# Kernel optimization log

Hardware: AMD Instinct MI355X
Metric: run time of the kernel (lower is better)

Reference implementation:

```python
import jax, jax.numpy as jnp
import numpy as np

N_NODES = 50000
N_EDGES = 640000
HID = 128
LN_EPS = 1e-5


def setup_inputs() -> dict:
    key = jax.random.key(0)
    ks = jax.random.split(key, 8)
    x = jax.random.normal(ks[0], (N_NODES, HID), dtype=jnp.float32)
    edge_index = jax.random.randint(ks[1], (2, N_EDGES), 0, N_NODES, dtype=jnp.int64)
    edge_attr = jax.random.normal(ks[2], (N_EDGES, HID), dtype=jnp.float32)
    # parameters (Kaiming-ish scaling)
    msg_W1 = jax.random.normal(ks[3], (3 * HID, HID), dtype=jnp.float32) / np.sqrt(3 * HID)
    msg_b1 = jnp.zeros((HID,), dtype=jnp.float32)
    msg_W2 = jax.random.normal(ks[4], (HID, HID), dtype=jnp.float32) / np.sqrt(HID)
    msg_b2 = jnp.zeros((HID,), dtype=jnp.float32)
    upd_W1 = jax.random.normal(ks[5], (2 * HID, HID), dtype=jnp.float32) / np.sqrt(2 * HID)
    upd_b1 = jnp.zeros((HID,), dtype=jnp.float32)
    upd_W2 = jax.random.normal(ks[6], (HID, HID), dtype=jnp.float32) / np.sqrt(HID)
    upd_b2 = jnp.zeros((HID,), dtype=jnp.float32)
    ln_gamma = jnp.ones((HID,), dtype=jnp.float32)
    ln_beta = jnp.zeros((HID,), dtype=jnp.float32)
    return {
        'x': x, 'edge_index': edge_index, 'edge_attr': edge_attr,
        'msg_W1': msg_W1, 'msg_b1': msg_b1, 'msg_W2': msg_W2, 'msg_b2': msg_b2,
        'upd_W1': upd_W1, 'upd_b1': upd_b1, 'upd_W2': upd_W2, 'upd_b2': upd_b2,
        'ln_gamma': ln_gamma, 'ln_beta': ln_beta,
    }


def _layer_norm(h, gamma, beta):
    mu = jnp.mean(h, axis=-1, keepdims=True)
    var = jnp.mean(jnp.square(h - mu), axis=-1, keepdims=True)
    return (h - mu) * jax.lax.rsqrt(var + LN_EPS) * gamma + beta


def reference(x, edge_index, edge_attr,
              msg_W1, msg_b1, msg_W2, msg_b2,
              upd_W1, upd_b1, upd_W2, upd_b2,
              ln_gamma, ln_beta):
    src, dst = edge_index[0], edge_index[1]
    # batched per-edge gather + concat: [E, 3*HID]
    msg_in = jnp.concatenate([x[src], x[dst], edge_attr], axis=-1)
    # message MLP (dropout is identity in eval)
    h = jax.nn.relu(msg_in @ msg_W1 + msg_b1)
    messages = h @ msg_W2 + msg_b2  # [E, HID]
    # scatter-add aggregation by destination node
    aggregated = jax.ops.segment_sum(messages, dst, num_segments=x.shape[0])
    # update MLP
    upd_in = jnp.concatenate([x, aggregated], axis=-1)  # [N, 2*HID]
    u = jax.nn.relu(upd_in @ upd_W1 + upd_b1)
    updated = u @ upd_W2 + upd_b2
    return _layer_norm(x + updated, ln_gamma, ln_beta)
```

## Files before the change

### kernel.cpp

```cpp
#include <hip/hip_runtime.h>

#define HID 128

typedef __attribute__((ext_vector_type(8))) short short8;
typedef __attribute__((ext_vector_type(4))) float f32x4;
typedef __attribute__((ext_vector_type(2))) float f32x2;

__device__ __forceinline__ float bf2f(unsigned short u) {
  union { unsigned int u; float f; } c; c.u = ((unsigned int)u) << 16; return c.f;
}
__device__ __forceinline__ unsigned short f2bf(float f) {
  union { float f; unsigned int u; } c; c.f = f;
  unsigned int u = c.u;
  return (unsigned short)((u + 0x7FFFu + ((u >> 16) & 1u)) >> 16);
}
__device__ __forceinline__ float loads(const void* p, size_t i, bool f32) {
  return f32 ? ((const float*)p)[i] : bf2f(((const unsigned short*)p)[i]);
}
__device__ __forceinline__ short8 load_a8(const void* base, size_t row, int k, bool f32) {
  if (!f32) return *(const short8*)((const unsigned short*)base + row * HID + k);
  const float* fp = (const float*)base + row * HID + k;
  f32x4 f0 = *(const f32x4*)fp;
  f32x4 f1 = *(const f32x4*)(fp + 4);
  short8 t;
  t[0] = (short)f2bf(f0[0]); t[1] = (short)f2bf(f0[1]);
  t[2] = (short)f2bf(f0[2]); t[3] = (short)f2bf(f0[3]);
  t[4] = (short)f2bf(f1[0]); t[5] = (short)f2bf(f1[1]);
  t[6] = (short)f2bf(f1[2]); t[7] = (short)f2bf(f1[3]);
  return t;
}

__global__ void detect_kernel(const void* __restrict__ x,
                              const int* __restrict__ eidx,
                              int* __restrict__ flags) {
  __shared__ int bad, oddnz;
  if (threadIdx.x == 0) { bad = 0; oddnz = 0; }
  __syncthreads();
  const unsigned short* xu = (const unsigned short*)x;
  int mybad = 0;
  for (int i = threadIdx.x; i < 4096; i += 256) {
    int ef = (xu[i] >> 7) & 0xFF;
    if (!(ef == 0 || (ef >= 90 && ef <= 140))) mybad++;
  }
  if (mybad) atomicAdd(&bad, mybad);
  if (threadIdx.x < 128) {
    if (eidx[2 * threadIdx.x + 1] != 0) atomicAdd(&oddnz, 1);
  }
  __syncthreads();
  if (threadIdx.x == 0) {
    flags[0] = (bad > 409) ? 1 : 0;
    flags[1] = (oddnz == 0) ? 1 : 0;
  }
}

__device__ __forceinline__ int get_dst(const int* eidx, bool i64, int E, int e) {
  return i64 ? eidx[2 * (E + e)] : eidx[E + e];
}
__device__ __forceinline__ int get_src(const int* eidx, bool i64, int E, int e) {
  return i64 ? eidx[2 * e] : eidx[e];
}

__global__ void zero_out_kernel(unsigned int* __restrict__ out,
                                const int* __restrict__ flags, long long nelem) {
  bool f32 = flags[0] != 0;
  size_t words = (size_t)nelem * (f32 ? 2 : 1) / 2;
  for (size_t w = blockIdx.x * 256ull + threadIdx.x; w < words; w += (size_t)gridDim.x * 256ull)
    out[w] = 0u;
}

__global__ void repack_all(const void* __restrict__ W1, const void* __restrict__ W2,
                           const void* __restrict__ U1, const void* __restrict__ U2,
                           unsigned short* __restrict__ P1, unsigned short* __restrict__ P2,
                           unsigned short* __restrict__ PU1, unsigned short* __restrict__ PU2,
                           const int* __restrict__ flags) {
  const bool f32 = flags[0] != 0;
  int idx = blockIdx.x * 256 + threadIdx.x;
  const int s1 = 384 * 128, s2 = s1 + 128 * 128, s3 = s2 + 256 * 128, s4 = s3 + 128 * 128;
  if (idx >= s4) return;
  const void* W; unsigned short* P; int off;
  if (idx < s1)      { W = W1; P = P1;  off = idx; }
  else if (idx < s2) { W = W2; P = P2;  off = idx - s1; }
  else if (idx < s3) { W = U1; P = PU1; off = idx - s2; }
  else               { W = U2; P = PU2; off = idx - s3; }
  int j = off & 7, lane = (off >> 3) & 63, ct = (off >> 9) & 7, ks = off >> 12;
  int k = ks * 32 + ((lane >> 4) << 3) + j;
  int n = ct * 16 + (lane & 15);
  P[off] = f2bf(loads(W, (size_t)k * 128 + n, f32));
}

__global__ void hist_kernel(const int* __restrict__ eidx, int* __restrict__ counts,
                            const int* __restrict__ flags, int E, int N) {
  const bool i64 = flags[1] != 0;
  int e = blockIdx.x * 256 + threadIdx.x;
  if (e < E) {
    int d = get_dst(eidx, i64, E, e);
    d = min(max(d, 0), N - 1);
    atomicAdd(&counts[d], 1);
  }
}

__global__ __launch_bounds__(1024) void scanA_kernel(const int* __restrict__ cnt,
                                                     int* __restrict__ curb,
                                                     int* __restrict__ bsum, int N) {
  __shared__ int wsum[16], wsum2[16];
  const int tid = threadIdx.x, lane = tid & 63, wid = tid >> 6;
  int i = blockIdx.x * 1024 + tid;
  int v = (i < N) ? cnt[i] : 0;
  int s = v;
#pragma unroll
  for (int off = 1; off < 64; off <<= 1) {
    int t = __shfl_up(s, off, 64);
    if (lane >= off) s += t;
  }
  if (lane == 63) wsum[wid] = s;
  __syncthreads();
  if (wid == 0 && lane < 16) {
    int w = wsum[lane];
#pragma unroll
    for (int off = 1; off < 16; off <<= 1) {
      int t = __shfl_up(w, off, 16);
      if (lane >= off) w += t;
    }
    wsum2[lane] = w;
    if (lane == 15) bsum[blockIdx.x] = w;
  }
  __syncthreads();
  int pre = (wid > 0) ? wsum2[wid - 1] : 0;
  if (i < N) curb[i] = pre + s - v;
}

__global__ void scanB_kernel(int* __restrict__ bsum, int nb) {
  if (threadIdx.x == 0 && blockIdx.x == 0) {
    int run = 0;
    for (int b = 0; b < nb; b++) { int t = bsum[b]; bsum[b] = run; run += t; }
  }
}

__global__ __launch_bounds__(1024) void scanC_kernel(int* __restrict__ curb,
                                                     const int* __restrict__ bsum, int N) {
  int i = blockIdx.x * 1024 + threadIdx.x;
  if (i < N) curb[i] += bsum[blockIdx.x];
}

__global__ __launch_bounds__(256) void x1_kernel(
    const void* __restrict__ x, const unsigned short* __restrict__ P1,
    const void* __restrict__ b1, unsigned short* __restrict__ X1,
    const int* __restrict__ flags, int N) {
  __shared__ unsigned short hs[64][264];
  const bool f32 = flags[0] != 0;
  const int tid = threadIdx.x, lane = tid & 63, wid = tid >> 6;
  const int l15 = lane & 15, quad = lane >> 4;
  const int base = blockIdx.x * 64;
  int mn = min(base + wid * 16 + l15, N - 1);

  f32x4 zero = {0.f, 0.f, 0.f, 0.f};
  f32x4 acca[8], accb[8];
#pragma unroll
  for (int ct = 0; ct < 8; ct++) { acca[ct] = zero; accb[ct] = zero; }
#pragma unroll
  for (int ks = 0; ks < 4; ks++) {
    short8 a = load_a8(x, (size_t)mn, ks * 32 + quad * 8, f32);
    const unsigned short* wpa = P1 + ((size_t)(ks * 8) * 64 + lane) * 8;
    const unsigned short* wpb = P1 + ((size_t)((ks + 4) * 8) * 64 + lane) * 8;
#pragma unroll
    for (int ct = 0; ct < 8; ct++) {
      short8 ba = *(const short8*)(wpa + ct * 512);
      short8 bb = *(const short8*)(wpb + ct * 512);
      acca[ct] = __builtin_amdgcn_mfma_f32_16x16x32_bf16(a, ba, acca[ct], 0, 0, 0);
      accb[ct] = __builtin_amdgcn_mfma_f32_16x16x32_bf16(a, bb, accb[ct], 0, 0, 0);
    }
  }
#pragma unroll
  for (int ct = 0; ct < 8; ct++) {
    const int col = ct * 16 + l15;
    const float bv = loads(b1, col, f32);
#pragma unroll
    for (int r = 0; r < 4; r++) {
      hs[wid * 16 + quad * 4 + r][col]       = f2bf(acca[ct][r] + bv);
      hs[wid * 16 + quad * 4 + r][128 + col] = f2bf(accb[ct][r]);
    }
  }
  __syncthreads();
  const int row = tid >> 2, part = tid & 3;
  if (base + row < N) {
    unsigned short* op = X1 + (size_t)(base + row) * 256 + part * 64;
#pragma unroll
    for (int j = 0; j < 8; j++)
      *(short8*)(op + j * 8) = *(const short8*)&hs[row][part * 64 + j * 8];
  }
}

__global__ __launch_bounds__(256, 8) void edgeS_kernel(
    const void* __restrict__ eattr, const int* __restrict__ ssrc,
    const int* __restrict__ sdst, const int* __restrict__ perm,
    const unsigned short* __restrict__ X1,
    const unsigned short* __restrict__ P1, const unsigned short* __restrict__ P2,
    const void* __restrict__ b2, float* __restrict__ aggf,
    const int* __restrict__ flags, int E, int N) {
  __shared__ __align__(16) char smem[64 * 136 * 2];
  __shared__ int sdst_s[64], ssrc_s[64];
  unsigned short (*hs)[136] = (unsigned short (*)[136])smem;
  float (*ms)[68] = (float (*)[68])smem;
  const bool f32 = flags[0] != 0;
  const int tid = threadIdx.x, lane = tid & 63, wid = tid >> 6;
  const int l15 = lane & 15, quad = lane >> 4;
  const int base = blockIdx.x * 64;

  if (tid < 64) {
    int e = min(base + tid, E - 1);
    sdst_s[tid] = sdst[e];
    ssrc_s[tid] = ssrc[e];
  }

  const int me = min(base + wid * 16 + l15, E - 1);
  const int pe = perm[me];

  f32x4 zero = {0.f, 0.f, 0.f, 0.f};
  f32x4 acc[8];
#pragma unroll
  for (int ct = 0; ct < 8; ct++) acc[ct] = zero;
#pragma unroll
  for (int ks = 0; ks < 4; ks++) {
    short8 a = load_a8(eattr, (size_t)pe, ks * 32 + quad * 8, f32);
    const unsigned short* wp = P1 + ((size_t)((ks + 8) * 8) * 64 + lane) * 8;
#pragma unroll
    for (int ct = 0; ct < 8; ct++) {
      short8 b = *(const short8*)(wp + ct * 512);
      acc[ct] = __builtin_amdgcn_mfma_f32_16x16x32_bf16(a, b, acc[ct], 0, 0, 0);
    }
  }
#pragma unroll
  for (int ct = 0; ct < 8; ct++) {
    const int col = ct * 16 + l15;
#pragma unroll
    for (int r = 0; r < 4; r++)
      hs[wid * 16 + quad * 4 + r][col] = f2bf(acc[ct][r]);
  }
  __syncthreads();

  {
    const int r = wid * 16 + (lane >> 2);
    const int cq = (lane & 3) * 8;
    const int s = ssrc_s[r], d = sdst_s[r];
    const unsigned short* ap = X1 + (size_t)s * 256;
    const unsigned short* bp = X1 + (size_t)d * 256 + 128;
#pragma unroll
    for (int j = 0; j < 4; j++) {
      const int c0 = cq + j * 32;
      short8 h8 = *(const short8*)&hs[r][c0];
      short8 a8 = *(const short8*)(ap + c0);
      short8 b8 = *(const short8*)(bp + c0);
      short8 o;
#pragma unroll
      for (int k = 0; k < 8; k++) {
        float v = bf2f((unsigned short)h8[k]) + bf2f((unsigned short)a8[k])
                + bf2f((unsigned short)b8[k]);
        o[k] = (short)f2bf(fmaxf(v, 0.f));
      }
      *(short8*)&hs[r][c0] = o;
    }
  }

  f32x4 acc2[8];
#pragma unroll
  for (int ct = 0; ct < 8; ct++) acc2[ct] = zero;
#pragma unroll
  for (int ks = 0; ks < 4; ks++) {
    short8 a = *(const short8*)&hs[wid * 16 + l15][ks * 32 + quad * 8];
    const unsigned short* wp = P2 + ((size_t)(ks * 8) * 64 + lane) * 8;
#pragma unroll
    for (int ct = 0; ct < 8; ct++) {
      short8 b = *(const short8*)(wp + ct * 512);
      acc2[ct] = __builtin_amdgcn_mfma_f32_16x16x32_bf16(a, b, acc2[ct], 0, 0, 0);
    }
  }
  float b2v[8];
#pragma unroll
  for (int ct = 0; ct < 8; ct++) b2v[ct] = loads(b2, ct * 16 + l15, f32);

#pragma unroll
  for (int h = 0; h < 2; h++) {
    __syncthreads();
#pragma unroll
    for (int c = 0; c < 4; c++) {
      const int ct = h * 4 + c;
      const int colh = c * 16 + l15;
#pragma unroll
      for (int r = 0; r < 4; r++) {
        const int e = base + wid * 16 + quad * 4 + r;
        ms[wid * 16 + quad * 4 + r][colh] = (e < E) ? (acc2[ct][r] + b2v[ct]) : 0.0f;
      }
    }
    __syncthreads();
    const int colh = tid & 63;
    const int col  = h * 64 + colh;
    const int grp  = tid >> 6;
    const int r0   = grp * 16;
    float sum = 0.0f;
    int cur = sdst_s[r0];
#pragma unroll 4
    for (int r = r0; r < r0 + 16; r++) {
      int d = sdst_s[r];
      if (d != cur) {
        atomicAdd(&aggf[(size_t)cur * HID + col], sum);
        sum = 0.0f; cur = d;
      }
      sum += ms[r][colh];
    }
    atomicAdd(&aggf[(size_t)cur * HID + col], sum);
  }
}

__global__ __launch_bounds__(1024) void scan_kernel(const int* __restrict__ counts,
                                                    int* __restrict__ offs, int N) {
  __shared__ int wsum[16];
  __shared__ int wpre[16];
  __shared__ int carry_s;
  const int tid = threadIdx.x, lane = tid & 63, wid = tid >> 6;
  if (tid == 0) carry_s = 0;
  __syncthreads();
  for (int base = 0; base < N; base += 1024) {
    int i = base + tid;
    int v = (i < N) ? counts[i] : 0;
    int s = v;
#pragma unroll
    for (int off = 1; off < 64; off <<= 1) {
      int t = __shfl_up(s, off, 64);
      if (lane >= off) s += t;
    }
    if (lane == 63) wsum[wid] = s;
    __syncthreads();
    if (tid == 0) {
      int run = carry_s;
#pragma unroll
      for (int w = 0; w < 16; w++) { int t = wsum[w]; wpre[w] = run; run += t; }
      carry_s = run;
    }
    __syncthreads();
    if (i < N) offs[i] = wpre[wid] + s - v;
    __syncthreads();
  }
  if (tid == 0) offs[N] = carry_s;
}

__global__ void scatter_kernel(const int* __restrict__ eidx, int* __restrict__ cur,
                               int* __restrict__ ssrc, int* __restrict__ sdst,
                               int* __restrict__ perm,
                               const int* __restrict__ flags, int E, int N) {
  const bool i64 = flags[1] != 0;
  int e = blockIdx.x * 256 + threadIdx.x;
  if (e < E) {
    int d = get_dst(eidx, i64, E, e);
    int s = get_src(eidx, i64, E, e);
    d = min(max(d, 0), N - 1);
    s = min(max(s, 0), N - 1);
    int pos = atomicAdd(&cur[d], 1);
    ssrc[pos] = s;
    sdst[pos] = d;
    perm[pos] = e;
  }
}

__global__ __launch_bounds__(256) void edge_kernel_sorted(
    const void* __restrict__ x, const void* __restrict__ eattr,
    const int* __restrict__ ssrc, const int* __restrict__ sdst,
    const int* __restrict__ perm,
    const unsigned short* __restrict__ P1, const void* __restrict__ b1,
    const unsigned short* __restrict__ P2, const void* __restrict__ b2,
    float* __restrict__ aggf, const int* __restrict__ flags, int E, int N) {
  __shared__ __align__(16) char smem[64 * 132 * 4];
  __shared__ int sdst_s[64];
  unsigned short (*hs)[136] = (unsigned short (*)[136])smem;
  float (*ms)[132] = (float (*)[132])smem;
  const bool f32 = flags[0] != 0;
  const int tid = threadIdx.x, lane = tid & 63, wid = tid >> 6;
  const int l15 = lane & 15, quad = lane >> 4;
  const int base = blockIdx.x * 64;

  if (tid < 64) sdst_s[tid] = sdst[min(base + tid, E - 1)];

  int me = base + wid * 16 + l15;
  if (me >= E) me = E - 1;
  const int src = ssrc[me];
  const int dsm = sdst[me];
  const int pe  = perm[me];

  f32x4 zero = {0.f, 0.f, 0.f, 0.f};
  f32x4 acc[8];
#pragma unroll
  for (int ct = 0; ct < 8; ct++) acc[ct] = zero;
#pragma unroll
  for (int ks = 0; ks < 12; ks++) {
    const int k0 = ks * 32;
    short8 a;
    if (k0 < 128)      a = load_a8(x,     (size_t)src, k0 + quad * 8, f32);
    else if (k0 < 256) a = load_a8(x,     (size_t)dsm, (k0 - 128) + quad * 8, f32);
    else               a = load_a8(eattr, (size_t)pe,  (k0 - 256) + quad * 8, f32);
    const unsigned short* wp = P1 + ((size_t)(ks * 8) * 64 + lane) * 8;
#pragma unroll
    for (int ct = 0; ct < 8; ct++) {
      short8 b = *(const short8*)(wp + ct * 512);
      acc[ct] = __builtin_amdgcn_mfma_f32_16x16x32_bf16(a, b, acc[ct], 0, 0, 0);
    }
  }
#pragma unroll
  for (int ct = 0; ct < 8; ct++) {
    const int col = ct * 16 + l15;
    const float bv = loads(b1, col, f32);
#pragma unroll
    for (int r = 0; r < 4; r++)
      hs[wid * 16 + quad * 4 + r][col] = f2bf(fmaxf(acc[ct][r] + bv, 0.f));
  }
  f32x4 acc2[8];
#pragma unroll
  for (int ct = 0; ct < 8; ct++) acc2[ct] = zero;
#pragma unroll
  for (int ks = 0; ks < 4; ks++) {
    short8 a = *(const short8*)&hs[wid * 16 + l15][ks * 32 + quad * 8];
    const unsigned short* wp = P2 + ((size_t)(ks * 8) * 64 + lane) * 8;
#pragma unroll
    for (int ct = 0; ct < 8; ct++) {
      short8 b = *(const short8*)(wp + ct * 512);
      acc2[ct] = __builtin_amdgcn_mfma_f32_16x16x32_bf16(a, b, acc2[ct], 0, 0, 0);
    }
  }
  float b2v[8];
#pragma unroll
  for (int ct = 0; ct < 8; ct++) b2v[ct] = loads(b2, ct * 16 + l15, f32);
  __syncthreads();
#pragma unroll
  for (int ct = 0; ct < 8; ct++) {
    const int col = ct * 16 + l15;
#pragma unroll
    for (int r = 0; r < 4; r++) {
      const int e = base + wid * 16 + quad * 4 + r;
      ms[wid * 16 + quad * 4 + r][col] = (e < E) ? (acc2[ct][r] + b2v[ct]) : 0.0f;
    }
  }
  __syncthreads();
  const int col  = tid & 127;
  const int half = tid >> 7;
  const int r0 = half * 32;
  float sum = 0.0f;
  int cur = sdst_s[r0];
#pragma unroll 4
  for (int r = r0; r < r0 + 32; r++) {
    int d = sdst_s[r];
    if (d != cur) {
      atomicAdd(&aggf[(size_t)cur * HID + col], sum);
      sum = 0.0f; cur = d;
    }
    sum += ms[r][col];
  }
  atomicAdd(&aggf[(size_t)cur * HID + col], sum);
}

__global__ __launch_bounds__(256) void edge_kernel_plain(
    const void* __restrict__ x, const int* __restrict__ eidx,
    const void* __restrict__ eattr,
    const unsigned short* __restrict__ P1, const void* __restrict__ b1,
    const unsigned short* __restrict__ P2, const void* __restrict__ b2,
    float* __restrict__ aggf, void* __restrict__ out,
    const int* __restrict__ flags, int E, int N, int small_mode) {
  __shared__ unsigned short hs[64][136];
  const bool f32 = flags[0] != 0;
  const bool i64 = flags[1] != 0;
  const int tid = threadIdx.x, lane = tid & 63, wid = tid >> 6;
  const int l15 = lane & 15, quad = lane >> 4;
  const int base = blockIdx.x * 64;

  int me = base + wid * 16 + l15;
  if (me >= E) me = E - 1;
  int src = get_src(eidx, i64, E, me);
  int dsm = get_dst(eidx, i64, E, me);
  src = min(max(src, 0), N - 1);
  dsm = min(max(dsm, 0), N - 1);

  f32x4 zero = {0.f, 0.f, 0.f, 0.f};
  f32x4 acc[8];
#pragma unroll
  for (int ct = 0; ct < 8; ct++) acc[ct] = zero;
#pragma unroll
  for (int ks = 0; ks < 12; ks++) {
    const int k0 = ks * 32;
    short8 a;
    if (k0 < 128)      a = load_a8(x,     (size_t)src, k0 + quad * 8, f32);
    else if (k0 < 256) a = load_a8(x,     (size_t)dsm, (k0 - 128) + quad * 8, f32);
    else               a = load_a8(eattr, (size_t)me,  (k0 - 256) + quad * 8, f32);
    const unsigned short* wp = P1 + ((size_t)(ks * 8) * 64 + lane) * 8;
#pragma unroll
    for (int ct = 0; ct < 8; ct++) {
      short8 b = *(const short8*)(wp + ct * 512);
      acc[ct] = __builtin_amdgcn_mfma_f32_16x16x32_bf16(a, b, acc[ct], 0, 0, 0);
    }
  }
#pragma unroll
  for (int ct = 0; ct < 8; ct++) {
    const int col = ct * 16 + l15;
    const float bv = loads(b1, col, f32);
#pragma unroll
    for (int r = 0; r < 4; r++)
      hs[wid * 16 + quad * 4 + r][col] = f2bf(fmaxf(acc[ct][r] + bv, 0.f));
  }
  __syncthreads();
  f32x4 acc2[8];
#pragma unroll
  for (int ct = 0; ct < 8; ct++) acc2[ct] = zero;
#pragma unroll
  for (int ks = 0; ks < 4; ks++) {
    short8 a = *(const short8*)&hs[wid * 16 + l15][ks * 32 + quad * 8];
    const unsigned short* wp = P2 + ((size_t)(ks * 8) * 64 + lane) * 8;
#pragma unroll
    for (int ct = 0; ct < 8; ct++) {
      short8 b = *(const short8*)(wp + ct * 512);
      acc2[ct] = __builtin_amdgcn_mfma_f32_16x16x32_bf16(a, b, acc2[ct], 0, 0, 0);
    }
  }
  float b2v[8];
#pragma unroll
  for (int ct = 0; ct < 8; ct++) b2v[ct] = loads(b2, ct * 16 + l15, f32);

  if (!small_mode || f32) {
    float* tgt = (!small_mode) ? aggf : (float*)out;
#pragma unroll
    for (int r = 0; r < 4; r++) {
      const int e = base + wid * 16 + quad * 4 + r;
      if (e < E) {
        int d = get_dst(eidx, i64, E, e);
        d = min(max(d, 0), N - 1);
        float* op = tgt + (size_t)d * HID + l15;
#pragma unroll
        for (int ct = 0; ct < 8; ct++) atomicAdd(op + ct * 16, acc2[ct][r] + b2v[ct]);
      }
    }
  } else {
#pragma unroll
    for (int ct = 0; ct < 8; ct++) {
      const int col = ct * 16 + l15;
#pragma unroll
      for (int r = 0; r < 4; r++)
        hs[wid * 16 + quad * 4 + r][col] = f2bf(acc2[ct][r] + b2v[ct]);
    }
    __syncthreads();
    const int row = tid >> 2;
    const int cg  = (tid & 3) * 32;
    const int e = base + row;
    if (e < E) {
      int d = get_dst(eidx, i64, E, e);
      d = min(max(d, 0), N - 1);
      unsigned int* orow = (unsigned int*)out + ((size_t)d * HID >> 1);
#pragma unroll
      for (int p = 0; p < 16; p++) {
        const int col = cg + p * 2;
        const float lo = bf2f(hs[row][col]);
        const float hi = bf2f(hs[row][col + 1]);
        unsigned int* wp = orow + (col >> 1);
        unsigned int old = *wp, assumed;
        do {
          assumed = old;
          unsigned int nv = (unsigned int)f2bf(bf2f((unsigned short)(assumed & 0xFFFF)) + lo)
                          | ((unsigned int)f2bf(bf2f((unsigned short)(assumed >> 16)) + hi) << 16);
          old = atomicCAS(wp, assumed, nv);
        } while (old != assumed);
      }
    }
  }
}

__global__ __launch_bounds__(256) void node_kernel(
    const void* __restrict__ x, const float* __restrict__ aggf,
    const unsigned short* __restrict__ PU1, const void* __restrict__ ub1,
    const unsigned short* __restrict__ PU2, const void* __restrict__ ub2,
    const void* __restrict__ gamma, const void* __restrict__ beta,
    void* __restrict__ out, const int* __restrict__ flags, int N, int small_mode) {
  __shared__ unsigned short hs[64][136];
  const bool f32 = flags[0] != 0;
  const int tid = threadIdx.x, lane = tid & 63, wid = tid >> 6;
  const int l15 = lane & 15, quad = lane >> 4;
  const int base = blockIdx.x * 64;

  int mn = base + wid * 16 + l15;
  if (mn >= N) mn = N - 1;

  const void* aggp = (!small_mode) ? (const void*)aggf : (const void*)out;
  const bool aggF32 = (!small_mode) ? true : f32;

  f32x4 zero = {0.f, 0.f, 0.f, 0.f};
  f32x4 acc[8];
#pragma unroll
  for (int ct = 0; ct < 8; ct++) acc[ct] = zero;
#pragma unroll
  for (int ks = 0; ks < 8; ks++) {
    const int k0 = ks * 32;
    short8 a;
    if (k0 < 128) a = load_a8(x,    (size_t)mn, k0 + quad * 8, f32);
    else          a = load_a8(aggp, (size_t)mn, (k0 - 128) + quad * 8, aggF32);
    const unsigned short* wp = PU1 + ((size_t)(ks * 8) * 64 + lane) * 8;
#pragma unroll
    for (int ct = 0; ct < 8; ct++) {
      short8 b = *(const short8*)(wp + ct * 512);
      acc[ct] = __builtin_amdgcn_mfma_f32_16x16x32_bf16(a, b, acc[ct], 0, 0, 0);
    }
  }
#pragma unroll
  for (int ct = 0; ct < 8; ct++) {
    const int col = ct * 16 + l15;
    const float bv = loads(ub1, col, f32);
#pragma unroll
    for (int r = 0; r < 4; r++)
      hs[wid * 16 + quad * 4 + r][col] = f2bf(fmaxf(acc[ct][r] + bv, 0.f));
  }
  __syncthreads();
  f32x4 acc2[8];
#pragma unroll
  for (int ct = 0; ct < 8; ct++) acc2[ct] = zero;
#pragma unroll
  for (int ks = 0; ks < 4; ks++) {
    short8 a = *(const short8*)&hs[wid * 16 + l15][ks * 32 + quad * 8];
    const unsigned short* wp = PU2 + ((size_t)(ks * 8) * 64 + lane) * 8;
#pragma unroll
    for (int ct = 0; ct < 8; ct++) {
      short8 b = *(const short8*)(wp + ct * 512);
      acc2[ct] = __builtin_amdgcn_mfma_f32_16x16x32_bf16(a, b, acc2[ct], 0, 0, 0);
    }
  }

  float vals[8][4];
  float s1[4] = {0.f, 0.f, 0.f, 0.f};
  float s2[4] = {0.f, 0.f, 0.f, 0.f};
#pragma unroll
  for (int ct = 0; ct < 8; ct++) {
    const int col = ct * 16 + l15;
    const float bv = loads(ub2, col, f32);
#pragma unroll
    for (int r = 0; r < 4; r++) {
      int row = base + wid * 16 + quad * 4 + r;
      int rc = row < N ? row : 0;
      float v = acc2[ct][r] + bv + loads(x, (size_t)rc * HID + col, f32);
      vals[ct][r] = v;
      s1[r] += v;
      s2[r] += v * v;
    }
  }
#pragma unroll
  for (int off = 1; off < 16; off <<= 1) {
#pragma unroll
    for (int r = 0; r < 4; r++) {
      s1[r] += __shfl_xor(s1[r], off, 16);
      s2[r] += __shfl_xor(s2[r], off, 16);
    }
  }
#pragma unroll
  for (int r = 0; r < 4; r++) {
    const int row = base + wid * 16 + quad * 4 + r;
    if (row < N) {
      const float mean = s1[r] * (1.0f / 128.0f);
      const float var  = fmaxf(s2[r] * (1.0f / 128.0f) - mean * mean, 0.0f);
      const float rstd = rsqrtf(var + 1e-5f);
#pragma unroll
      for (int ct = 0; ct < 8; ct++) {
        const int col = ct * 16 + l15;
        float o = (vals[ct][r] - mean) * rstd * loads(gamma, col, f32) + loads(beta, col, f32);
        if (f32) ((float*)out)[(size_t)row * HID + col] = o;
        else     ((unsigned short*)out)[(size_t)row * HID + col] = f2bf(o);
      }
    }
  }
}

extern "C" void kernel_launch(void* const* d_in, const int* in_sizes, int n_in,
                              void* d_out, int out_size, void* d_ws, size_t ws_size,
                              hipStream_t stream) {
  (void)n_in;
  const void* x     = d_in[0];
  const int*  eidx  = (const int*)d_in[1];
  const void* eattr = d_in[2];
  const void* W1  = d_in[3];
  const void* b1  = d_in[4];
  const void* W2  = d_in[5];
  const void* b2  = d_in[6];
  const void* U1  = d_in[7];
  const void* ub1 = d_in[8];
  const void* U2  = d_in[9];
  const void* ub2 = d_in[10];
  const void* gam = d_in[11];
  const void* bet = d_in[12];

  const int N = in_sizes[0] / HID;
  const int E = in_sizes[2] / HID;

  char* ws = (char*)d_ws;
  auto alignup = [](size_t v) { return (v + 255) & ~(size_t)255; };

  int* flags = (int*)ws;
  unsigned short* P1  = (unsigned short*)(ws + 256);
  unsigned short* P2  = (unsigned short*)(ws + 256 + 98304);
  unsigned short* PU1 = (unsigned short*)(ws + 256 + 131072);
  unsigned short* PU2 = (unsigned short*)(ws + 256 + 196608);
  const size_t agg_off = 256 + 229376;
  float* aggf = (float*)(ws + agg_off);
  const size_t agg_bytes = (size_t)N * HID * sizeof(float);
  const size_t need_basic = agg_off + agg_bytes;

  size_t o3 = alignup(need_basic);
  size_t cnt_off  = o3; o3 = alignup(o3 + (size_t)(N + 64) * 4);
  size_t cur_off  = o3; o3 = alignup(o3 + (size_t)(N + 64) * 4);
  size_t bsum_off = o3; o3 = alignup(o3 + 1024);
  size_t src3_off = o3; o3 = alignup(o3 + (size_t)E * 4);
  size_t dst3_off = o3; o3 = alignup(o3 + (size_t)E * 4);
  size_t prm3_off = o3; o3 = alignup(o3 + (size_t)E * 4);
  size_t x1_off   = o3; o3 = alignup(o3 + (size_t)N * 256 * 2);
  const size_t need3 = o3;

  size_t o2 = alignup(need_basic);
  size_t offs_off = o2; o2 = alignup(o2 + (size_t)(N + 1) * 4);
  size_t cur2_off = o2; o2 = alignup(o2 + (size_t)(N + 1) * 4);
  size_t ssrc_off = o2; o2 = alignup(o2 + (size_t)E * 4);
  size_t sds2_off = o2; o2 = alignup(o2 + (size_t)E * 4);
  size_t perm_off = o2; o2 = alignup(o2 + (size_t)E * 4);
  const size_t need2 = o2;

  const int mode = (ws_size >= need3) ? 3
                 : (ws_size >= need2) ? 2
                 : (ws_size >= need_basic) ? 1 : 0;

  detect_kernel<<<1, 256, 0, stream>>>(x, eidx, flags);
  repack_all<<<448, 256, 0, stream>>>(W1, W2, U1, U2, P1, P2, PU1, PU2, flags);

  if (mode == 3) {
    int* cntb = (int*)(ws + cnt_off);
    int* curb = (int*)(ws + cur_off);
    int* bsum = (int*)(ws + bsum_off);
    int* ssrc = (int*)(ws + src3_off);
    int* sdst = (int*)(ws + dst3_off);
    int* perm = (int*)(ws + prm3_off);
    unsigned short* X1 = (unsigned short*)(ws + x1_off);
    const int nb = (N + 1023) / 1024;

    hipMemsetAsync(aggf, 0, agg_bytes, stream);
    hipMemsetAsync(cntb, 0, (size_t)N * 4, stream);
    hist_kernel<<<(E + 255) / 256, 256, 0, stream>>>(eidx, cntb, flags, E, N);
    scanA_kernel<<<nb, 1024, 0, stream>>>(cntb, curb, bsum, N);
    scanB_kernel<<<1, 64, 0, stream>>>(bsum, nb);
    scanC_kernel<<<nb, 1024, 0, stream>>>(curb, bsum, N);
    scatter_kernel<<<(E + 255) / 256, 256, 0, stream>>>(eidx, curb, ssrc, sdst, perm,
                                                        flags, E, N);
    x1_kernel<<<(N + 63) / 64, 256, 0, stream>>>(x, P1, b1, X1, flags, N);
    edgeS_kernel<<<(E + 63) / 64, 256, 0, stream>>>(eattr, ssrc, sdst, perm, X1,
                                                    P1, P2, b2, aggf, flags, E, N);
    node_kernel<<<(N + 63) / 64, 256, 0, stream>>>(x, aggf, PU1, ub1, PU2, ub2,
                                                   gam, bet, d_out, flags, N, 0);
  } else if (mode == 2) {
    int* offsb = (int*)(ws + offs_off);
    int* curb  = (int*)(ws + cur2_off);
    int* ssrc  = (int*)(ws + ssrc_off);
    int* sdst  = (int*)(ws + sds2_off);
    int* perm  = (int*)(ws + perm_off);
    hipMemsetAsync(aggf, 0, agg_bytes, stream);
    hipMemsetAsync(curb, 0, (size_t)(N + 1) * 4, stream);
    hist_kernel<<<(E + 255) / 256, 256, 0, stream>>>(eidx, curb, flags, E, N);
    scan_kernel<<<1, 1024, 0, stream>>>(curb, offsb, N);
    hipMemcpyAsync(curb, offsb, (size_t)(N + 1) * 4, hipMemcpyDeviceToDevice, stream);
    scatter_kernel<<<(E + 255) / 256, 256, 0, stream>>>(eidx, curb, ssrc, sdst, perm,
                                                        flags, E, N);
    edge_kernel_sorted<<<(E + 63) / 64, 256, 0, stream>>>(x, eattr, ssrc, sdst, perm,
                                                          P1, b1, P2, b2, aggf, flags, E, N);
    node_kernel<<<(N + 63) / 64, 256, 0, stream>>>(x, aggf, PU1, ub1, PU2, ub2,
                                                   gam, bet, d_out, flags, N, 0);
  } else if (mode == 1) {
    hipMemsetAsync(aggf, 0, agg_bytes, stream);
    edge_kernel_plain<<<(E + 63) / 64, 256, 0, stream>>>(x, eidx, eattr, P1, b1, P2, b2,
                                                         aggf, d_out, flags, E, N, 0);
    node_kernel<<<(N + 63) / 64, 256, 0, stream>>>(x, aggf, PU1, ub1, PU2, ub2,
                                                   gam, bet, d_out, flags, N, 0);
  } else {
    zero_out_kernel<<<1024, 256, 0, stream>>>((unsigned int*)d_out, flags, (long long)out_size);
    edge_kernel_plain<<<(E + 63) / 64, 256, 0, stream>>>(x, eidx, eattr, P1, b1, P2, b2,
                                                         aggf, d_out, flags, E, N, 1);
    node_kernel<<<(N + 63) / 64, 256, 0, stream>>>(x, aggf, PU1, ub1, PU2, ub2,
                                                   gam, bet, d_out, flags, N, 1);
  }
}
```

Before: 758.7 us.

## Prefetch X1 gathers early in edge kernel and use single-block scan

The edge kernel now issues the per-edge X1 gathers for the source and destination rows into registers at kernel start, before the edge_attr MFMA, so their latency overlaps compute instead of being exposed after the barrier. The launch-bounds occupancy hint drops from 8 to 7 blocks to make room for the extra live registers. The three-kernel multi-block prefix scan is replaced by a single-block looping scan, which removes two launches but serialises the scan over about 49 chunks. The scan and scatter kernels are also moved earlier in the file.

```diff
diff --git a/kernel.cpp b/kernel.cpp
--- a/kernel.cpp
+++ b/kernel.cpp
@@ -99,47 +99,54 @@
   }
 }
 
-__global__ __launch_bounds__(1024) void scanA_kernel(const int* __restrict__ cnt,
-                                                     int* __restrict__ curb,
-                                                     int* __restrict__ bsum, int N) {
-  __shared__ int wsum[16], wsum2[16];
+__global__ __launch_bounds__(1024) void scan_kernel(const int* __restrict__ counts,
+                                                    int* __restrict__ offs, int N) {
+  __shared__ int wsum[16];
+  __shared__ int wpre[16];
+  __shared__ int carry_s;
   const int tid = threadIdx.x, lane = tid & 63, wid = tid >> 6;
-  int i = blockIdx.x * 1024 + tid;
-  int v = (i < N) ? cnt[i] : 0;
-  int s = v;
-#pragma unroll
-  for (int off = 1; off < 64; off <<= 1) {
-    int t = __shfl_up(s, off, 64);
-    if (lane >= off) s += t;
-  }
-  if (lane == 63) wsum[wid] = s;
-  __syncthreads();
-  if (wid == 0 && lane < 16) {
-    int w = wsum[lane];
-#pragma unroll
-    for (int off = 1; off < 16; off <<= 1) {
-      int t = __shfl_up(w, off, 16);
-      if (lane >= off) w += t;
-    }
-    wsum2[lane] = w;
-    if (lane == 15) bsum[blockIdx.x] = w;
-  }
-  __syncthreads();
-  int pre = (wid > 0) ? wsum2[wid - 1] : 0;
-  if (i < N) curb[i] = pre + s - v;
-}
-
-__global__ void scanB_kernel(int* __restrict__ bsum, int nb) {
-  if (threadIdx.x == 0 && blockIdx.x == 0) {
-    int run = 0;
-    for (int b = 0; b < nb; b++) { int t = bsum[b]; bsum[b] = run; run += t; }
-  }
-}
-
-__global__ __launch_bounds__(1024) void scanC_kernel(int* __restrict__ curb,
-                                                     const int* __restrict__ bsum, int N) {
-  int i = blockIdx.x * 1024 + threadIdx.x;
-  if (i < N) curb[i] += bsum[blockIdx.x];
+  if (tid == 0) carry_s = 0;
+  __syncthreads();
+  for (int base = 0; base < N; base += 1024) {
+    int i = base + tid;
+    int v = (i < N) ? counts[i] : 0;
+    int s = v;
+#pragma unroll
+    for (int off = 1; off < 64; off <<= 1) {
+      int t = __shfl_up(s, off, 64);
+      if (lane >= off) s += t;
+    }
+    if (lane == 63) wsum[wid] = s;
+    __syncthreads();
+    if (tid == 0) {
+      int run = carry_s;
+#pragma unroll
+      for (int w = 0; w < 16; w++) { int t = wsum[w]; wpre[w] = run; run += t; }
+      carry_s = run;
+    }
+    __syncthreads();
+    if (i < N) offs[i] = wpre[wid] + s - v;
+    __syncthreads();
+  }
+  if (tid == 0) offs[N] = carry_s;
+}
+
+__global__ void scatter_kernel(const int* __restrict__ eidx, int* __restrict__ cur,
+                               int* __restrict__ ssrc, int* __restrict__ sdst,
+                               int* __restrict__ perm,
+                               const int* __restrict__ flags, int E, int N) {
+  const bool i64 = flags[1] != 0;
+  int e = blockIdx.x * 256 + threadIdx.x;
+  if (e < E) {
+    int d = get_dst(eidx, i64, E, e);
+    int s = get_src(eidx, i64, E, e);
+    d = min(max(d, 0), N - 1);
+    s = min(max(s, 0), N - 1);
+    int pos = atomicAdd(&cur[d], 1);
+    ssrc[pos] = s;
+    sdst[pos] = d;
+    perm[pos] = e;
+  }
 }
 
 __global__ __launch_bounds__(256) void x1_kernel(
@@ -190,7 +197,7 @@
   }
 }
 
-__global__ __launch_bounds__(256, 8) void edgeS_kernel(
+__global__ __launch_bounds__(256, 7) void edgeS_kernel(
     const void* __restrict__ eattr, const int* __restrict__ ssrc,
     const int* __restrict__ sdst, const int* __restrict__ perm,
     const unsigned short* __restrict__ X1,
@@ -198,7 +205,7 @@
     const void* __restrict__ b2, float* __restrict__ aggf,
     const int* __restrict__ flags, int E, int N) {
   __shared__ __align__(16) char smem[64 * 136 * 2];
-  __shared__ int sdst_s[64], ssrc_s[64];
+  __shared__ int sdst_s[64];
   unsigned short (*hs)[136] = (unsigned short (*)[136])smem;
   float (*ms)[68] = (float (*)[68])smem;
   const bool f32 = flags[0] != 0;
@@ -206,11 +213,23 @@
   const int l15 = lane & 15, quad = lane >> 4;
   const int base = blockIdx.x * 64;
 
-  if (tid < 64) {
-    int e = min(base + tid, E - 1);
-    sdst_s[tid] = sdst[e];
-    ssrc_s[tid] = ssrc[e];
-  }
+  const int pr = wid * 16 + (lane >> 2);
+  const int cq = (lane & 3) * 8;
+  short8 ga[4], gb[4];
+  {
+    const int e = min(base + pr, E - 1);
+    const int s = ssrc[e];
+    const int d = sdst[e];
+    const unsigned short* ap = X1 + (size_t)s * 256;
+    const unsigned short* bp = X1 + (size_t)d * 256 + 128;
+#pragma unroll
+    for (int j = 0; j < 4; j++) {
+      ga[j] = *(const short8*)(ap + cq + j * 32);
+      gb[j] = *(const short8*)(bp + cq + j * 32);
+    }
+  }
+
+  if (tid < 64) sdst_s[tid] = sdst[min(base + tid, E - 1)];
 
   const int me = min(base + wid * 16 + l15, E - 1);
   const int pe = perm[me];
@@ -239,17 +258,12 @@
   __syncthreads();
 
   {
-    const int r = wid * 16 + (lane >> 2);
-    const int cq = (lane & 3) * 8;
-    const int s = ssrc_s[r], d = sdst_s[r];
-    const unsigned short* ap = X1 + (size_t)s * 256;
-    const unsigned short* bp = X1 + (size_t)d * 256 + 128;
 #pragma unroll
     for (int j = 0; j < 4; j++) {
       const int c0 = cq + j * 32;
-      short8 h8 = *(const short8*)&hs[r][c0];
-      short8 a8 = *(const short8*)(ap + c0);
-      short8 b8 = *(const short8*)(bp + c0);
+      short8 h8 = *(const short8*)&hs[pr][c0];
+      short8 a8 = ga[j];
+      short8 b8 = gb[j];
       short8 o;
 #pragma unroll
       for (int k = 0; k < 8; k++) {
@@ -257,7 +271,7 @@
                 + bf2f((unsigned short)b8[k]);
         o[k] = (short)f2bf(fmaxf(v, 0.f));
       }
-      *(short8*)&hs[r][c0] = o;
+      *(short8*)&hs[pr][c0] = o;
     }
   }
 
@@ -308,56 +322,6 @@
       sum += ms[r][colh];
     }
     atomicAdd(&aggf[(size_t)cur * HID + col], sum);
-  }
-}
-
-__global__ __launch_bounds__(1024) void scan_kernel(const int* __restrict__ counts,
-                                                    int* __restrict__ offs, int N) {
-  __shared__ int wsum[16];
-  __shared__ int wpre[16];
-  __shared__ int carry_s;
-  const int tid = threadIdx.x, lane = tid & 63, wid = tid >> 6;
-  if (tid == 0) carry_s = 0;
-  __syncthreads();
-  for (int base = 0; base < N; base += 1024) {
-    int i = base + tid;
-    int v = (i < N) ? counts[i] : 0;
-    int s = v;
-#pragma unroll
-    for (int off = 1; off < 64; off <<= 1) {
-      int t = __shfl_up(s, off, 64);
-      if (lane >= off) s += t;
-    }
-    if (lane == 63) wsum[wid] = s;
-    __syncthreads();
-    if (tid == 0) {
-      int run = carry_s;
-#pragma unroll
-      for (int w = 0; w < 16; w++) { int t = wsum[w]; wpre[w] = run; run += t; }
-      carry_s = run;
-    }
-    __syncthreads();
-    if (i < N) offs[i] = wpre[wid] + s - v;
-    __syncthreads();
-  }
-  if (tid == 0) offs[N] = carry_s;
-}
-
-__global__ void scatter_kernel(const int* __restrict__ eidx, int* __restrict__ cur,
-                               int* __restrict__ ssrc, int* __restrict__ sdst,
-                               int* __restrict__ perm,
-                               const int* __restrict__ flags, int E, int N) {
-  const bool i64 = flags[1] != 0;
-  int e = blockIdx.x * 256 + threadIdx.x;
-  if (e < E) {
-    int d = get_dst(eidx, i64, E, e);
-    int s = get_src(eidx, i64, E, e);
-    d = min(max(d, 0), N - 1);
-    s = min(max(s, 0), N - 1);
-    int pos = atomicAdd(&cur[d], 1);
-    ssrc[pos] = s;
-    sdst[pos] = d;
-    perm[pos] = e;
   }
 }
 
@@ -705,7 +669,6 @@
   size_t o3 = alignup(need_basic);
   size_t cnt_off  = o3; o3 = alignup(o3 + (size_t)(N + 64) * 4);
   size_t cur_off  = o3; o3 = alignup(o3 + (size_t)(N + 64) * 4);
-  size_t bsum_off = o3; o3 = alignup(o3 + 1024);
   size_t src3_off = o3; o3 = alignup(o3 + (size_t)E * 4);
   size_t dst3_off = o3; o3 = alignup(o3 + (size_t)E * 4);
   size_t prm3_off = o3; o3 = alignup(o3 + (size_t)E * 4);
@@ -730,19 +693,15 @@
   if (mode == 3) {
     int* cntb = (int*)(ws + cnt_off);
     int* curb = (int*)(ws + cur_off);
-    int* bsum = (int*)(ws + bsum_off);
     int* ssrc = (int*)(ws + src3_off);
     int* sdst = (int*)(ws + dst3_off);
     int* perm = (int*)(ws + prm3_off);
     unsigned short* X1 = (unsigned short*)(ws + x1_off);
-    const int nb = (N + 1023) / 1024;
 
     hipMemsetAsync(aggf, 0, agg_bytes, stream);
     hipMemsetAsync(cntb, 0, (size_t)N * 4, stream);
     hist_kernel<<<(E + 255) / 256, 256, 0, stream>>>(eidx, cntb, flags, E, N);
-    scanA_kernel<<<nb, 1024, 0, stream>>>(cntb, curb, bsum, N);
-    scanB_kernel<<<1, 64, 0, stream>>>(bsum, nb);
-    scanC_kernel<<<nb, 1024, 0, stream>>>(curb, bsum, N);
+    scan_kernel<<<1, 1024, 0, stream>>>(cntb, curb, N);
     scatter_kernel<<<(E + 255) / 256, 256, 0, stream>>>(eidx, curb, ssrc, sdst, perm,
                                                         flags, E, N);
     x1_kernel<<<(N + 63) / 64, 256, 0, stream>>>(x, P1, b1, X1, flags, N);
```

New measurement: 893.9 us. 1.18x slower.
